# Performance work log

Hardware: AMD Instinct MI355X
Metric: run time of the kernel (lower is better)

Reference implementation:

```python
import jax, jax.numpy as jnp
import numpy as np

IOU_T = 0.5          # iou_threshold
SCORE_T = 0.5        # score_threshold
MAX_OUT = 100        # max_output_boxes_per_class


def setup_inputs() -> dict:
    key = jax.random.key(0)
    k1, k2, k3 = jax.random.split(key, 3)
    B, C, N = 1, 80, 1024
    # boxes in y1x1y2x2 with positive extents (realistic detector outputs)
    mins = jax.random.uniform(k1, (B, N, 2), jnp.float32) * 100.0
    sizes = jax.random.uniform(k2, (B, N, 2), jnp.float32) * 50.0 + 1.0
    boxes = jnp.concatenate([mins, mins + sizes], axis=-1)  # [B, N, 4]
    scores = jax.random.uniform(k3, (B, C, N), jnp.float32)  # [B, C, N]
    return {"boxes": boxes, "scores": scores}


def _pairwise_iou(b):
    # b: [N,4] in y1x1y2x2 (IoU is invariant to the module's axis swap)
    y1, x1, y2, x2 = b[:, 0], b[:, 1], b[:, 2], b[:, 3]
    area = (y2 - y1) * (x2 - x1)
    ih = jnp.clip(jnp.minimum(y2[:, None], y2[None, :]) - jnp.maximum(y1[:, None], y1[None, :]), 0.0)
    iw = jnp.clip(jnp.minimum(x2[:, None], x2[None, :]) - jnp.maximum(x1[:, None], x1[None, :]), 0.0)
    inter = ih * iw
    return inter / (area[:, None] + area[None, :] - inter)


def _nms_one_class(boxes, scores):
    # boxes: [N,4], scores: [N] -> (idx:[MAX_OUT] kept original indices, -1 pad; valid:[MAX_OUT])
    N = scores.shape[0]
    order = jnp.argsort(-scores)              # descending score, matches torchvision.nms
    iou = _pairwise_iou(boxes[order])         # [N,N] in sorted order
    keep = scores[order] > SCORE_T            # score filter folded into initial keep mask
    js = jnp.arange(N)

    def body(i, keep):
        suppress = (iou[i] > IOU_T) & (js > i)
        return jnp.where(keep[i], keep & ~suppress, keep)

    keep = jax.lax.fori_loop(0, N, body, keep)
    rank = jnp.cumsum(keep) - 1               # output slot for each kept box
    slots = jnp.where(keep, jnp.clip(rank, 0, MAX_OUT), MAX_OUT)  # MAX_OUT = discard slot
    res = jnp.full((MAX_OUT + 1,), -1, jnp.int32).at[slots].set(order.astype(jnp.int32))
    idx = res[:MAX_OUT]
    return idx, idx >= 0


def reference(boxes, scores):
    B, C = scores.shape[0], scores.shape[1]
    nms_bc = jax.vmap(jax.vmap(_nms_one_class, in_axes=(None, 0)), in_axes=(0, 0))
    idx, valid = nms_bc(boxes, scores)        # [B,C,MAX_OUT]
    b_idx = jnp.broadcast_to(jnp.arange(B, dtype=jnp.int32)[:, None, None], (B, C, MAX_OUT))
    c_idx = jnp.broadcast_to(jnp.arange(C, dtype=jnp.int32)[None, :, None], (B, C, MAX_OUT))
    rows = jnp.stack([b_idx, c_idx, idx], axis=-1).reshape(-1, 3)  # [B*C*MAX_OUT, 3]
    v = valid.reshape(-1)
    total = B * C * MAX_OUT
    # pack valid rows contiguously at the front (mirrors torch's put_ on a zeros buffer)
    pos = jnp.where(v, jnp.cumsum(v.astype(jnp.int32)) - 1, total)
    out = jnp.zeros((total, 3), jnp.int32).at[pos].set(rows, mode='drop')
    return out
```

## Files before the change

### kernel.cpp

```cpp
#include <hip/hip_runtime.h>
#include <stdint.h>

#define N_BOX 1024
#define NUM_CLASSES 80
#define MAX_OUT 100

__device__ __forceinline__ void cas64(unsigned long long& a, unsigned long long& b, bool desc) {
    bool sw = desc ? (a < b) : (a > b);
    unsigned long long t = a;
    a = sw ? b : a;
    b = sw ? t : b;
}

__global__ __launch_bounds__(256) void nms_class_kernel(const float* __restrict__ boxes,
                                                        const float* __restrict__ scores,
                                                        int* __restrict__ keptIdx,
                                                        int* __restrict__ counts) {
    __shared__ float4 sbox[N_BOX];
    __shared__ float sarea[N_BOX];
    __shared__ unsigned long long keys[N_BOX];
    __shared__ float4 kbox[MAX_OUT];
    __shared__ float karea[MAX_OUT];
    const int c = blockIdx.x;
    const int tid = threadIdx.x;
    const int lane = tid & 63;

    for (int i = tid; i < N_BOX; i += 256) {
        float4 b = reinterpret_cast<const float4*>(boxes)[i];
        sbox[i] = b;
        sarea[i] = (b.z - b.x) * (b.w - b.y);
    }

    const float* sc = scores + (size_t)c * N_BOX;
    float4 s4 = reinterpret_cast<const float4*>(sc)[tid];
    const int i0 = tid * 4;
    unsigned long long K[4];
    K[0] = ((unsigned long long)__float_as_uint(s4.x) << 32) | (unsigned long long)(0xFFFFFFFFu - (unsigned)(i0 + 0));
    K[1] = ((unsigned long long)__float_as_uint(s4.y) << 32) | (unsigned long long)(0xFFFFFFFFu - (unsigned)(i0 + 1));
    K[2] = ((unsigned long long)__float_as_uint(s4.z) << 32) | (unsigned long long)(0xFFFFFFFFu - (unsigned)(i0 + 2));
    K[3] = ((unsigned long long)__float_as_uint(s4.w) << 32) | (unsigned long long)(0xFFFFFFFFu - (unsigned)(i0 + 3));

    auto shfl_pass = [&](int j, bool d) {
        int xl = j >> 2;
        bool mx = (d == ((lane & xl) == 0));
#pragma unroll
        for (int t = 0; t < 4; ++t) {
            unsigned long long p = __shfl_xor(K[t], xl, 64);
            K[t] = mx ? (K[t] >= p ? K[t] : p) : (K[t] <= p ? K[t] : p);
        }
    };
    auto thread_pass = [&](bool d) {
        cas64(K[0], K[2], d); cas64(K[1], K[3], d);
        cas64(K[0], K[1], d); cas64(K[2], K[3], d);
    };
    auto lds_pass = [&](int j, bool d) {
        *reinterpret_cast<ulonglong2*>(&keys[i0])     = make_ulonglong2(K[0], K[1]);
        *reinterpret_cast<ulonglong2*>(&keys[i0 + 2]) = make_ulonglong2(K[2], K[3]);
        __syncthreads();
        int pb = i0 ^ j;
        ulonglong2 p01 = *reinterpret_cast<const ulonglong2*>(&keys[pb]);
        ulonglong2 p23 = *reinterpret_cast<const ulonglong2*>(&keys[pb + 2]);
        unsigned long long P[4] = {p01.x, p01.y, p23.x, p23.y};
        bool mx = (d == ((i0 & j) == 0));
#pragma unroll
        for (int t = 0; t < 4; ++t)
            K[t] = mx ? (K[t] >= P[t] ? K[t] : P[t]) : (K[t] <= P[t] ? K[t] : P[t]);
        __syncthreads();
    };

    cas64(K[0], K[1], true);
    cas64(K[2], K[3], false);
    { bool d = (tid & 1) == 0; thread_pass(d); }
    for (int k = 8; k <= 256; k <<= 1) {
        bool d = (tid & (k >> 2)) == 0;
        for (int j = k >> 1; j >= 4; j >>= 1) shfl_pass(j, d);
        thread_pass(d);
    }
    { bool d = (tid & 128) == 0;
      lds_pass(256, d);
      for (int j = 128; j >= 4; j >>= 1) shfl_pass(j, d);
      thread_pass(d); }
    {
      lds_pass(512, true); lds_pass(256, true);
      for (int j = 128; j >= 4; j >>= 1) shfl_pass(j, true);
      thread_pass(true); }
    *reinterpret_cast<ulonglong2*>(&keys[i0])     = make_ulonglong2(K[0], K[1]);
    *reinterpret_cast<ulonglong2*>(&keys[i0 + 2]) = make_ulonglong2(K[2], K[3]);
    __syncthreads();

    if (tid < 64) {
        int kept = 0;
        int* outc = keptIdx + c * MAX_OUT;
        for (int base = 0; base < N_BOX && kept < MAX_OUT; base += 64) {
            unsigned long long kk = keys[base + lane];
            unsigned int hi = (unsigned int)(kk >> 32);
            unsigned int o = 0xFFFFFFFFu - (unsigned int)kk;
            bool valid = hi > 0x3F000000u;
            if (__ballot(valid) == 0ull) break;
            float4 mb = sbox[o];
            float ma = sarea[o];
            bool alive = valid;
            for (int j = 0; j < kept; ++j) {
                float4 kb = kbox[j];
                float ih = fminf(kb.z, mb.z) - fmaxf(kb.x, mb.x); ih = fmaxf(ih, 0.0f);
                float iw = fminf(kb.w, mb.w) - fmaxf(kb.y, mb.y); iw = fmaxf(iw, 0.0f);
                float inter = ih * iw;
                float uni = karea[j] + ma - inter;
                alive = alive && !((inter / uni) > 0.5f);
            }
            unsigned long long m = __ballot(alive);
            while (m != 0ull && kept < MAX_OUT) {
                int f = __builtin_ctzll(m);
                float fx = __shfl(mb.x, f), fy = __shfl(mb.y, f);
                float fz = __shfl(mb.z, f), fw = __shfl(mb.w, f);
                float fa = __shfl(ma, f);
                unsigned int of = (unsigned int)__shfl((int)o, f);
                float ih = fminf(fz, mb.z) - fmaxf(fx, mb.x); ih = fmaxf(ih, 0.0f);
                float iw = fminf(fw, mb.w) - fmaxf(fy, mb.y); iw = fmaxf(iw, 0.0f);
                float inter = ih * iw;
                float uni = fa + ma - inter;
                bool sup = (inter / uni) > 0.5f;
                if (lane == 0) {
                    outc[kept] = (int)of;
                    kbox[kept] = make_float4(fx, fy, fz, fw);
                    karea[kept] = fa;
                }
                ++kept;
                m &= ~__ballot(sup);
            }
        }
        if (lane == 0) counts[c] = kept;
    }
}

__global__ __launch_bounds__(256) void compact_kernel(const int* __restrict__ keptIdx,
                                                      const int* __restrict__ counts,
                                                      int* __restrict__ out) {
    int4* o4 = reinterpret_cast<int4*>(out);
    for (int i = threadIdx.x; i < (NUM_CLASSES * MAX_OUT * 3) / 4; i += 256)
        o4[i] = make_int4(0, 0, 0, 0);
    __shared__ int offs[NUM_CLASSES + 1];
    if (threadIdx.x == 0) {
        int s = 0;
        for (int c = 0; c < NUM_CLASSES; ++c) { offs[c] = s; s += counts[c]; }
        offs[NUM_CLASSES] = s;
    }
    __syncthreads();
    for (int idx = threadIdx.x; idx < NUM_CLASSES * MAX_OUT; idx += 256) {
        int c = idx / MAX_OUT;
        int r = idx - c * MAX_OUT;
        int o0 = offs[c];
        if (r < offs[c + 1] - o0) {
            int o = o0 + r;
            out[o * 3 + 0] = 0;
            out[o * 3 + 1] = c;
            out[o * 3 + 2] = keptIdx[c * MAX_OUT + r];
        }
    }
}

extern "C" void kernel_launch(void* const* d_in, const int* in_sizes, int n_in,
                              void* d_out, int out_size, void* d_ws, size_t ws_size,
                              hipStream_t stream) {
    const float* boxes = (const float*)d_in[0];
    const float* scores = (const float*)d_in[1];
    int* out = (int*)d_out;

    int* keptIdx = (int*)d_ws;
    int* counts = keptIdx + NUM_CLASSES * MAX_OUT;

    nms_class_kernel<<<NUM_CLASSES, 256, 0, stream>>>(boxes, scores, keptIdx, counts);
    compact_kernel<<<1, 256, 0, stream>>>(keptIdx, counts, out);
}
```

Measured before the change: 103.1 us.

## Split sort and greedy NMS into separate kernels with intra-chunk suppression bitmask

Splits the fused per-class kernel into a bitonic sort kernel that writes sorted keys to global workspace and a 64-thread greedy kernel that reads them back. The greedy kernel now builds a 64-bit suppression mask for each chunk in parallel, then resolves kept boxes with readlane and bit operations, instead of issuing one shuffle and one ballot per kept box. The aim is to shorten the serial dependency chain inside each chunk and to give the greedy stage a small block. The cost is an extra kernel launch, a global round trip for the keys, and 64 IoU evaluations per lane per chunk even when few boxes survive.

```diff
diff --git a/kernel.cpp b/kernel.cpp
--- a/kernel.cpp
+++ b/kernel.cpp
@@ -4,6 +4,7 @@
 #define N_BOX 1024
 #define NUM_CLASSES 80
 #define MAX_OUT 100
+#define KEPT_STRIDE 128
 
 __device__ __forceinline__ void cas64(unsigned long long& a, unsigned long long& b, bool desc) {
     bool sw = desc ? (a < b) : (a > b);
@@ -12,24 +13,12 @@
     b = sw ? t : b;
 }
 
-__global__ __launch_bounds__(256) void nms_class_kernel(const float* __restrict__ boxes,
-                                                        const float* __restrict__ scores,
-                                                        int* __restrict__ keptIdx,
-                                                        int* __restrict__ counts) {
-    __shared__ float4 sbox[N_BOX];
-    __shared__ float sarea[N_BOX];
+__global__ __launch_bounds__(256) void sort_kernel(const float* __restrict__ scores,
+                                                   unsigned long long* __restrict__ gkeys) {
     __shared__ unsigned long long keys[N_BOX];
-    __shared__ float4 kbox[MAX_OUT];
-    __shared__ float karea[MAX_OUT];
     const int c = blockIdx.x;
     const int tid = threadIdx.x;
     const int lane = tid & 63;
-
-    for (int i = tid; i < N_BOX; i += 256) {
-        float4 b = reinterpret_cast<const float4*>(boxes)[i];
-        sbox[i] = b;
-        sarea[i] = (b.z - b.x) * (b.w - b.y);
-    }
 
     const float* sc = scores + (size_t)c * N_BOX;
     float4 s4 = reinterpret_cast<const float4*>(sc)[tid];
@@ -80,61 +69,93 @@
       lds_pass(256, d);
       for (int j = 128; j >= 4; j >>= 1) shfl_pass(j, d);
       thread_pass(d); }
-    {
-      lds_pass(512, true); lds_pass(256, true);
+    { lds_pass(512, true); lds_pass(256, true);
       for (int j = 128; j >= 4; j >>= 1) shfl_pass(j, true);
       thread_pass(true); }
-    *reinterpret_cast<ulonglong2*>(&keys[i0])     = make_ulonglong2(K[0], K[1]);
-    *reinterpret_cast<ulonglong2*>(&keys[i0 + 2]) = make_ulonglong2(K[2], K[3]);
-    __syncthreads();
 
-    if (tid < 64) {
-        int kept = 0;
-        int* outc = keptIdx + c * MAX_OUT;
-        for (int base = 0; base < N_BOX && kept < MAX_OUT; base += 64) {
-            unsigned long long kk = keys[base + lane];
-            unsigned int hi = (unsigned int)(kk >> 32);
-            unsigned int o = 0xFFFFFFFFu - (unsigned int)kk;
-            bool valid = hi > 0x3F000000u;
-            if (__ballot(valid) == 0ull) break;
-            float4 mb = sbox[o];
-            float ma = sarea[o];
-            bool alive = valid;
-            for (int j = 0; j < kept; ++j) {
-                float4 kb = kbox[j];
-                float ih = fminf(kb.z, mb.z) - fmaxf(kb.x, mb.x); ih = fmaxf(ih, 0.0f);
-                float iw = fminf(kb.w, mb.w) - fmaxf(kb.y, mb.y); iw = fmaxf(iw, 0.0f);
-                float inter = ih * iw;
-                float uni = karea[j] + ma - inter;
-                alive = alive && !((inter / uni) > 0.5f);
-            }
-            unsigned long long m = __ballot(alive);
-            while (m != 0ull && kept < MAX_OUT) {
-                int f = __builtin_ctzll(m);
-                float fx = __shfl(mb.x, f), fy = __shfl(mb.y, f);
-                float fz = __shfl(mb.z, f), fw = __shfl(mb.w, f);
-                float fa = __shfl(ma, f);
-                unsigned int of = (unsigned int)__shfl((int)o, f);
-                float ih = fminf(fz, mb.z) - fmaxf(fx, mb.x); ih = fmaxf(ih, 0.0f);
-                float iw = fminf(fw, mb.w) - fmaxf(fy, mb.y); iw = fmaxf(iw, 0.0f);
-                float inter = ih * iw;
-                float uni = fa + ma - inter;
-                bool sup = (inter / uni) > 0.5f;
-                if (lane == 0) {
-                    outc[kept] = (int)of;
-                    kbox[kept] = make_float4(fx, fy, fz, fw);
-                    karea[kept] = fa;
-                }
-                ++kept;
-                m &= ~__ballot(sup);
-            }
+    unsigned long long* gk = gkeys + (size_t)c * N_BOX;
+    *reinterpret_cast<ulonglong2*>(&gk[i0])     = make_ulonglong2(K[0], K[1]);
+    *reinterpret_cast<ulonglong2*>(&gk[i0 + 2]) = make_ulonglong2(K[2], K[3]);
+}
+
+__global__ __launch_bounds__(64) void greedy_kernel(const float* __restrict__ boxes,
+                                                    const unsigned long long* __restrict__ gkeys,
+                                                    int* __restrict__ keptIdx,
+                                                    unsigned int* __restrict__ counts) {
+    __shared__ float4 sbox[N_BOX];
+    __shared__ float sarea[N_BOX];
+    __shared__ unsigned long long keys[N_BOX];
+    const int c = blockIdx.x;
+    const int lane = threadIdx.x;
+
+    for (int i = lane; i < N_BOX; i += 64) {
+        float4 b = reinterpret_cast<const float4*>(boxes)[i];
+        sbox[i] = b;
+        sarea[i] = (b.z - b.x) * (b.w - b.y);
+        keys[i] = gkeys[(size_t)c * N_BOX + i];
+    }
+
+    int kept = 0;
+    int* outc = keptIdx + c * KEPT_STRIDE;
+    float4 kbox[MAX_OUT > 0 ? 2 : 1];
+    (void)kbox;
+    __shared__ float4 kb_s[MAX_OUT];
+    __shared__ float ka_s[MAX_OUT];
+
+    for (int base = 0; base < N_BOX && kept < MAX_OUT; base += 64) {
+        unsigned long long kk = keys[base + lane];
+        unsigned int hi = (unsigned int)(kk >> 32);
+        unsigned int o = 0xFFFFFFFFu - (unsigned int)kk;
+        bool valid = hi > 0x3F000000u;
+        if (__ballot(valid) == 0ull) break;
+        float4 mb = sbox[o];
+        float ma = sarea[o];
+        bool alive = valid;
+        for (int j = 0; j < kept; ++j) {
+            float4 kb = kb_s[j];
+            float ih = fminf(kb.z, mb.z) - fmaxf(kb.x, mb.x); ih = fmaxf(ih, 0.0f);
+            float iw = fminf(kb.w, mb.w) - fmaxf(kb.y, mb.y); iw = fmaxf(iw, 0.0f);
+            float inter = ih * iw;
+            float uni = ka_s[j] + ma - inter;
+            alive = alive && !((inter / uni) > 0.5f);
         }
-        if (lane == 0) counts[c] = kept;
+        unsigned long long m = __ballot(alive);
+        if (m == 0ull) continue;
+        unsigned long long row = 0ull;
+#pragma unroll 8
+        for (int j = 0; j < 64; ++j) {
+            unsigned int oj = (unsigned int)__shfl((int)o, j);
+            float4 bj = sbox[oj];
+            float aj = sarea[oj];
+            float ih = fminf(bj.z, mb.z) - fmaxf(bj.x, mb.x); ih = fmaxf(ih, 0.0f);
+            float iw = fminf(bj.w, mb.w) - fmaxf(bj.y, mb.y); iw = fmaxf(iw, 0.0f);
+            float inter = ih * iw;
+            float uni = aj + ma - inter;
+            if ((inter / uni) > 0.5f) row |= 1ull << j;
+        }
+        unsigned long long Km = 0ull;
+        int kept0 = kept;
+        while (m != 0ull && kept < MAX_OUT) {
+            int f = __builtin_ctzll(m);
+            Km |= 1ull << f;
+            ++kept;
+            unsigned int rlo = (unsigned int)__builtin_amdgcn_readlane((int)(unsigned int)row, f);
+            unsigned int rhi = (unsigned int)__builtin_amdgcn_readlane((int)(unsigned int)(row >> 32), f);
+            unsigned long long rowf = ((unsigned long long)rhi << 32) | rlo;
+            m &= ~rowf;
+        }
+        if ((Km >> lane) & 1ull) {
+            int pos = kept0 + __popcll(Km & ((1ull << lane) - 1ull));
+            outc[pos] = (int)o;
+            kb_s[pos] = mb;
+            ka_s[pos] = ma;
+        }
     }
+    if (lane == 0) counts[c] = (unsigned int)kept;
 }
 
 __global__ __launch_bounds__(256) void compact_kernel(const int* __restrict__ keptIdx,
-                                                      const int* __restrict__ counts,
+                                                      const unsigned int* __restrict__ counts,
                                                       int* __restrict__ out) {
     int4* o4 = reinterpret_cast<int4*>(out);
     for (int i = threadIdx.x; i < (NUM_CLASSES * MAX_OUT * 3) / 4; i += 256)
@@ -142,7 +163,7 @@
     __shared__ int offs[NUM_CLASSES + 1];
     if (threadIdx.x == 0) {
         int s = 0;
-        for (int c = 0; c < NUM_CLASSES; ++c) { offs[c] = s; s += counts[c]; }
+        for (int c = 0; c < NUM_CLASSES; ++c) { offs[c] = s; s += (int)counts[c]; }
         offs[NUM_CLASSES] = s;
     }
     __syncthreads();
@@ -154,7 +175,7 @@
             int o = o0 + r;
             out[o * 3 + 0] = 0;
             out[o * 3 + 1] = c;
-            out[o * 3 + 2] = keptIdx[c * MAX_OUT + r];
+            out[o * 3 + 2] = keptIdx[c * KEPT_STRIDE + r];
         }
     }
 }
@@ -166,9 +187,11 @@
     const float* scores = (const float*)d_in[1];
     int* out = (int*)d_out;
 
-    int* keptIdx = (int*)d_ws;
-    int* counts = keptIdx + NUM_CLASSES * MAX_OUT;
+    unsigned long long* gkeys = (unsigned long long*)d_ws;
+    int* keptIdx = (int*)(gkeys + (size_t)NUM_CLASSES * N_BOX);
+    unsigned int* counts = (unsigned int*)(keptIdx + NUM_CLASSES * KEPT_STRIDE);
 
-    nms_class_kernel<<<NUM_CLASSES, 256, 0, stream>>>(boxes, scores, keptIdx, counts);
+    sort_kernel<<<NUM_CLASSES, 256, 0, stream>>>(scores, gkeys);
+    greedy_kernel<<<NUM_CLASSES, 64, 0, stream>>>(boxes, gkeys, keptIdx, counts);
     compact_kernel<<<1, 256, 0, stream>>>(keptIdx, counts, out);
 }
```

After: 106.5 us. 1.03x slower.
